# Performance work log

Hardware: AMD Instinct MI355X
Metric: run time of the kernel (lower is better)

Reference implementation:

```python
import jax, jax.numpy as jnp
import numpy as np

N_CLUSTERS = 16
N_ITERATIONS = 5
COV_INIT = 1.0


def setup_inputs() -> dict:
    key = jax.random.key(0)
    k1, k2 = jax.random.split(key)
    B, T, F, D = 8, 400, 256, 64
    data = jax.random.normal(k1, (B, T, F, D), dtype=jnp.float32)
    # Replicate init_means: per batch row, pick K random indices in [0, T),
    # offset by b*T, and gather rows of data flattened over (B,T,F).
    idx = jax.random.randint(k2, (B, N_CLUSTERS), 0, T)  # [B,K]
    idx = idx + jnp.arange(B)[:, None] * T
    flat = data.reshape(-1, D)  # [B*T*F, D]
    means = flat[idx.reshape(-1)].reshape(B, N_CLUSTERS, D)
    scale = jnp.ones((1,), dtype=jnp.float32)
    bias = jnp.zeros((1,), dtype=jnp.float32)
    return {"data": data, "means": means, "scale": scale, "bias": bias}


def _log_likelihoods(x, x2, means, var, pi):
    # x: [B,N,D], means/var: [B,K,D], pi: [B,K] -> lik: [B,K,N]
    inv = 1.0 / (var + 1e-6)
    # sum_d (x - m)^2 * inv, expanded into GEMM-friendly contractions
    dist = (jnp.einsum('bnd,bkd->bkn', x2, inv)
            - 2.0 * jnp.einsum('bnd,bkd->bkn', x, means * inv)
            + jnp.sum(means * means * inv, axis=-1)[:, :, None])
    coeff = -0.5 * jnp.sum(jnp.log(2.0 * np.pi * var), axis=-1)  # [B,K]
    return jnp.log(pi)[:, :, None] + coeff[:, :, None] - 0.5 * dist


def reference(data, means, scale, bias):
    B, T, F, D = data.shape
    K = means.shape[1]
    N = T * F
    x = data.reshape(B, N, D)
    x2 = x * x
    var = jnp.full((B, K, D), COV_INIT, dtype=data.dtype)
    pi = jnp.full((B, K), 1.0 / K, dtype=data.dtype)

    for _ in range(N_ITERATIONS):
        lik = _log_likelihoods(x, x2, means, var, pi)          # [B,K,N]
        post = jax.nn.softmax(lik, axis=1)                     # [B,K,N]
        cs = jnp.sum(post, axis=2)                             # [B,K]
        pi = cs / jnp.sum(cs, axis=1, keepdims=True)           # L1-normalized
        sx = jnp.einsum('bkn,bnd->bkd', post, x)               # [B,K,D]
        means = sx / (cs[:, :, None] + 1e-7)
        sx2 = jnp.einsum('bkn,bnd->bkd', post, x2)
        # sum_n post*(x - m)^2 = S(x^2) - 2 m S(x) + m^2 * cluster_size
        var = sx2 - 2.0 * means * sx + means * means * cs[:, :, None]
        var = var + 1e-6

    lik = _log_likelihoods(x, x2, means, var, pi)              # [B,K,N]
    lik = jnp.transpose(lik, (0, 2, 1)).reshape(B, T, F, K)
    return jax.nn.sigmoid(lik * scale[0] + bias[0])
```

## Files before the change

kernel.cpp:

```cpp
#include <hip/hip_runtime.h>
#include <math.h>

#define B_  8
#define T_  400
#define F_  256
#define D_  64
#define K_  16
#define N_  (T_*F_)
#define TILE 512
#define NBLK (N_/TILE)
#define PSTRIDE 20


__global__ void initk(const float* __restrict__ means_in,
                      float* __restrict__ means_s, float* __restrict__ var_s,
                      float* __restrict__ pi_s) {
    int i = blockIdx.x * 256 + threadIdx.x;
    if (i < B_*K_*D_) { means_s[i] = means_in[i]; var_s[i] = 1.0f; }
    if (i < B_*K_)    pi_s[i] = 1.0f / K_;
}

__global__ void prepk(const float* __restrict__ means_s, const float* __restrict__ var_s,
                      const float* __restrict__ pi_s,
                      float* __restrict__ pinv, float* __restrict__ pw,
                      float* __restrict__ pc0) {
    int bk = blockIdx.x;
    int d  = threadIdx.x;
    int idx = bk * D_ + d;
    float var = var_s[idx];
    float m   = means_s[idx];
    float inv = 1.0f / (var + 1e-6f);
    pinv[idx] = inv;
    pw[idx]   = m * inv;
    float r1 = logf(6.283185307179586f * var);
    float r2 = m * m * inv;
    #pragma unroll
    for (int off = 32; off > 0; off >>= 1) {
        r1 += __shfl_xor(r1, off);
        r2 += __shfl_xor(r2, off);
    }
    if (d == 0) pc0[bk] = logf(pi_s[bk]) - 0.5f * (r1 + r2);
}

__global__ __launch_bounds__(256, 3) void estepk(
        const float* __restrict__ xg,
        const float* __restrict__ pinv, const float* __restrict__ pw,
        const float* __restrict__ pc0,
        float* __restrict__ cs, float* __restrict__ sx, float* __restrict__ sx2) {
    __shared__ float pinv_lds[K_*D_];
    __shared__ float pw_lds[K_*D_];
    __shared__ float c0_lds[K_];
    __shared__ float post_lds[TILE * PSTRIDE];

    const int t  = threadIdx.x;
    const int b  = blockIdx.y;
    const int n0 = blockIdx.x * TILE;

    for (int i = t; i < K_*D_; i += 256) {
        pinv_lds[i] = pinv[b*K_*D_ + i];
        pw_lds[i]   = pw[b*K_*D_ + i];
    }
    if (t < K_) c0_lds[t] = pc0[b*K_ + t];
    __syncthreads();

    float t1a[16], t2a[16], t1b[16], t2b[16];
    #pragma unroll
    for (int k = 0; k < 16; ++k) { t1a[k]=0.f; t2a[k]=0.f; t1b[k]=0.f; t2b[k]=0.f; }

    const float4* pa = (const float4*)(xg + ((size_t)b*N_ + n0 + t) * D_);
    const float4* pb = pa + 256 * (D_/4);
    const float4* iv4 = (const float4*)pinv_lds;
    const float4* wv4 = (const float4*)pw_lds;

    #pragma unroll 2
    for (int c = 0; c < D_/4; ++c) {
        float4 xa = pa[c], xb = pb[c];
        float4 qa, qb;
        qa.x = xa.x*xa.x; qa.y = xa.y*xa.y; qa.z = xa.z*xa.z; qa.w = xa.w*xa.w;
        qb.x = xb.x*xb.x; qb.y = xb.y*xb.y; qb.z = xb.z*xb.z; qb.w = xb.w*xb.w;
        #pragma unroll
        for (int k = 0; k < 16; ++k) {
            float4 iv = iv4[k*16 + c];
            float4 wv = wv4[k*16 + c];
            t2a[k] = fmaf(qa.x, iv.x, fmaf(qa.y, iv.y, fmaf(qa.z, iv.z, fmaf(qa.w, iv.w, t2a[k]))));
            t1a[k] = fmaf(xa.x, wv.x, fmaf(xa.y, wv.y, fmaf(xa.z, wv.z, fmaf(xa.w, wv.w, t1a[k]))));
            t2b[k] = fmaf(qb.x, iv.x, fmaf(qb.y, iv.y, fmaf(qb.z, iv.z, fmaf(qb.w, iv.w, t2b[k]))));
            t1b[k] = fmaf(xb.x, wv.x, fmaf(xb.y, wv.y, fmaf(xb.z, wv.z, fmaf(xb.w, wv.w, t1b[k]))));
        }
    }

    {
        float lik[16]; float mx = -1e30f;
        #pragma unroll
        for (int k = 0; k < 16; ++k) { lik[k] = c0_lds[k] + t1a[k] - 0.5f*t2a[k]; mx = fmaxf(mx, lik[k]); }
        float s = 0.f;
        #pragma unroll
        for (int k = 0; k < 16; ++k) { lik[k] = __expf(lik[k] - mx); s += lik[k]; }
        float is = 1.0f / s;
        #pragma unroll
        for (int k = 0; k < 16; ++k) post_lds[t*PSTRIDE + k] = lik[k] * is;
    }
    {
        float lik[16]; float mx = -1e30f;
        #pragma unroll
        for (int k = 0; k < 16; ++k) { lik[k] = c0_lds[k] + t1b[k] - 0.5f*t2b[k]; mx = fmaxf(mx, lik[k]); }
        float s = 0.f;
        #pragma unroll
        for (int k = 0; k < 16; ++k) { lik[k] = __expf(lik[k] - mx); s += lik[k]; }
        float is = 1.0f / s;
        #pragma unroll
        for (int k = 0; k < 16; ++k) post_lds[(256 + t)*PSTRIDE + k] = lik[k] * is;
    }
    __syncthreads();

    const int lane = t & 63;
    const int kb   = (t >> 6) * 4;
    float sa[4]  = {0.f,0.f,0.f,0.f};
    float s2a[4] = {0.f,0.f,0.f,0.f};
    float ca[4]  = {0.f,0.f,0.f,0.f};
    const float* xrow = xg + ((size_t)b*N_ + n0) * D_ + lane;
    #pragma unroll 4
    for (int n = 0; n < TILE; ++n) {
        float xv = xrow[(size_t)n * D_];
        float4 p = *(const float4*)&post_lds[n*PSTRIDE + kb];
        float xx = xv * xv;
        ca[0] += p.x; ca[1] += p.y; ca[2] += p.z; ca[3] += p.w;
        sa[0] = fmaf(p.x, xv, sa[0]);  sa[1] = fmaf(p.y, xv, sa[1]);
        sa[2] = fmaf(p.z, xv, sa[2]);  sa[3] = fmaf(p.w, xv, sa[3]);
        s2a[0] = fmaf(p.x, xx, s2a[0]); s2a[1] = fmaf(p.y, xx, s2a[1]);
        s2a[2] = fmaf(p.z, xx, s2a[2]); s2a[3] = fmaf(p.w, xx, s2a[3]);
    }
    #pragma unroll
    for (int i = 0; i < 4; ++i) {
        atomicAdd(&sx [((size_t)b*K_ + kb + i)*D_ + lane], sa[i]);
        atomicAdd(&sx2[((size_t)b*K_ + kb + i)*D_ + lane], s2a[i]);
    }
    if (lane == 0) {
        #pragma unroll
        for (int i = 0; i < 4; ++i) atomicAdd(&cs[b*K_ + kb + i], ca[i]);
    }
}

__global__ void mstepk(float* __restrict__ means_s, float* __restrict__ var_s,
                       float* __restrict__ pi_s,
                       const float* __restrict__ cs, const float* __restrict__ sx,
                       const float* __restrict__ sx2) {
    int idx = blockIdx.x * 256 + threadIdx.x;
    int b = idx >> 10;
    int k = (idx >> 6) & 15;
    int d = idx & 63;
    float csv = cs[b*K_ + k];
    float sum = 0.f;
    #pragma unroll
    for (int j = 0; j < 16; ++j) sum += cs[b*K_ + j];
    float sxv = sx[idx], sx2v = sx2[idx];
    float mean = sxv / (csv + 1e-7f);
    float var  = fmaf(mean*mean, csv, fmaf(-2.0f*mean, sxv, sx2v)) + 1e-6f;
    means_s[idx] = mean;
    var_s[idx]   = var;
    if (d == 0) pi_s[b*K_ + k] = csv / sum;
}

__global__ __launch_bounds__(256, 3) void finalk(
        const float* __restrict__ xg,
        const float* __restrict__ pinv, const float* __restrict__ pw,
        const float* __restrict__ pc0,
        const float* __restrict__ scale, const float* __restrict__ bias,
        float* __restrict__ out) {
    __shared__ float pinv_lds[K_*D_];
    __shared__ float pw_lds[K_*D_];
    __shared__ float c0_lds[K_];

    const int t  = threadIdx.x;
    const int b  = blockIdx.y;
    const int n0 = blockIdx.x * TILE;

    for (int i = t; i < K_*D_; i += 256) {
        pinv_lds[i] = pinv[b*K_*D_ + i];
        pw_lds[i]   = pw[b*K_*D_ + i];
    }
    if (t < K_) c0_lds[t] = pc0[b*K_ + t];
    __syncthreads();

    float t1a[16], t2a[16], t1b[16], t2b[16];
    #pragma unroll
    for (int k = 0; k < 16; ++k) { t1a[k]=0.f; t2a[k]=0.f; t1b[k]=0.f; t2b[k]=0.f; }

    const float4* pa = (const float4*)(xg + ((size_t)b*N_ + n0 + t) * D_);
    const float4* pb = pa + 256 * (D_/4);
    const float4* iv4 = (const float4*)pinv_lds;
    const float4* wv4 = (const float4*)pw_lds;

    #pragma unroll 2
    for (int c = 0; c < D_/4; ++c) {
        float4 xa = pa[c], xb = pb[c];
        float4 qa, qb;
        qa.x = xa.x*xa.x; qa.y = xa.y*xa.y; qa.z = xa.z*xa.z; qa.w = xa.w*xa.w;
        qb.x = xb.x*xb.x; qb.y = xb.y*xb.y; qb.z = xb.z*xb.z; qb.w = xb.w*xb.w;
        #pragma unroll
        for (int k = 0; k < 16; ++k) {
            float4 iv = iv4[k*16 + c];
            float4 wv = wv4[k*16 + c];
            t2a[k] = fmaf(qa.x, iv.x, fmaf(qa.y, iv.y, fmaf(qa.z, iv.z, fmaf(qa.w, iv.w, t2a[k]))));
            t1a[k] = fmaf(xa.x, wv.x, fmaf(xa.y, wv.y, fmaf(xa.z, wv.z, fmaf(xa.w, wv.w, t1a[k]))));
            t2b[k] = fmaf(qb.x, iv.x, fmaf(qb.y, iv.y, fmaf(qb.z, iv.z, fmaf(qb.w, iv.w, t2b[k]))));
            t1b[k] = fmaf(xb.x, wv.x, fmaf(xb.y, wv.y, fmaf(xb.z, wv.z, fmaf(xb.w, wv.w, t1b[k]))));
        }
    }

    const float sc = scale[0], bi = bias[0];

    {
        float4* op = (float4*)(out + ((size_t)b*N_ + n0 + t) * (size_t)K_);
        #pragma unroll
        for (int q = 0; q < 4; ++q) {
            float4 o;
            float z0 = (c0_lds[4*q+0] + t1a[4*q+0] - 0.5f*t2a[4*q+0]) * sc + bi;
            float z1 = (c0_lds[4*q+1] + t1a[4*q+1] - 0.5f*t2a[4*q+1]) * sc + bi;
            float z2 = (c0_lds[4*q+2] + t1a[4*q+2] - 0.5f*t2a[4*q+2]) * sc + bi;
            float z3 = (c0_lds[4*q+3] + t1a[4*q+3] - 0.5f*t2a[4*q+3]) * sc + bi;
            o.x = 1.0f / (1.0f + __expf(-z0));
            o.y = 1.0f / (1.0f + __expf(-z1));
            o.z = 1.0f / (1.0f + __expf(-z2));
            o.w = 1.0f / (1.0f + __expf(-z3));
            op[q] = o;
        }
    }
    {
        float4* op = (float4*)(out + ((size_t)b*N_ + n0 + 256 + t) * (size_t)K_);
        #pragma unroll
        for (int q = 0; q < 4; ++q) {
            float4 o;
            float z0 = (c0_lds[4*q+0] + t1b[4*q+0] - 0.5f*t2b[4*q+0]) * sc + bi;
            float z1 = (c0_lds[4*q+1] + t1b[4*q+1] - 0.5f*t2b[4*q+1]) * sc + bi;
            float z2 = (c0_lds[4*q+2] + t1b[4*q+2] - 0.5f*t2b[4*q+2]) * sc + bi;
            float z3 = (c0_lds[4*q+3] + t1b[4*q+3] - 0.5f*t2b[4*q+3]) * sc + bi;
            o.x = 1.0f / (1.0f + __expf(-z0));
            o.y = 1.0f / (1.0f + __expf(-z1));
            o.z = 1.0f / (1.0f + __expf(-z2));
            o.w = 1.0f / (1.0f + __expf(-z3));
            op[q] = o;
        }
    }
}

extern "C" void kernel_launch(void* const* d_in, const int* in_sizes, int n_in,
                              void* d_out, int out_size, void* d_ws, size_t ws_size,
                              hipStream_t stream) {
    const float* xg       = (const float*)d_in[0];
    const float* means_in = (const float*)d_in[1];
    const float* scale    = (const float*)d_in[2];
    const float* bias     = (const float*)d_in[3];
    float* out = (float*)d_out;

    float* ws      = (float*)d_ws;
    float* means_s = ws + 0;
    float* var_s   = ws + 8192;
    float* pi_s    = ws + 16384;
    float* pinv    = ws + 16512;
    float* pw      = ws + 24704;
    float* pc0     = ws + 32896;
    float* cs      = ws + 33024;
    float* sx      = ws + 33152;
    float* sx2     = ws + 41344;

    initk<<<dim3(32), dim3(256), 0, stream>>>(means_in, means_s, var_s, pi_s);

    for (int it = 0; it < 5; ++it) {
        prepk<<<dim3(B_*K_), dim3(64), 0, stream>>>(means_s, var_s, pi_s, pinv, pw, pc0);
        hipMemsetAsync(cs, 0, (size_t)(128 + 8192 + 8192) * sizeof(float), stream);
        estepk<<<dim3(NBLK, B_), dim3(256), 0, stream>>>(xg, pinv, pw, pc0, cs, sx, sx2);
        mstepk<<<dim3(32), dim3(256), 0, stream>>>(means_s, var_s, pi_s, cs, sx, sx2);
    }
    prepk<<<dim3(B_*K_), dim3(64), 0, stream>>>(means_s, var_s, pi_s, pinv, pw, pc0);
    finalk<<<dim3(NBLK, B_), dim3(256), 0, stream>>>(xg, pinv, pw, pc0, scale, bias, out);
}
```

Baseline: 1.927 ms.

## Read cluster params from global memory and vectorize M-step accumulation with register tiling

The E-step and final kernels now read the per-batch inverse-variance and weighted-mean tables straight from global memory (uniform across the block, likely scalar or cache loads) instead of staging them in LDS, and keep the cluster constants in registers. Launch bounds rise to 4 blocks per SIMD. The accumulation phase now loads float4 rows of x, so each lane covers 4 dims by 4 clusters over strided rows, then combines partials with cross-lane shuffles before the atomics. This cuts LDS traffic and scalar global loads, at the cost of more registers and a shuffle reduction.

Result: faster. 1.733 ms (-10.1%).

```diff
diff --git a/kernel.cpp b/kernel.cpp
--- a/kernel.cpp
+++ b/kernel.cpp
@@ -9,7 +9,6 @@
 #define N_  (T_*F_)
 #define TILE 512
 #define NBLK (N_/TILE)
-#define PSTRIDE 20
 
 
 __global__ void initk(const float* __restrict__ means_in,
@@ -42,26 +41,23 @@
     if (d == 0) pc0[bk] = logf(pi_s[bk]) - 0.5f * (r1 + r2);
 }
 
-__global__ __launch_bounds__(256, 3) void estepk(
+__global__ __launch_bounds__(256, 4) void estepk(
         const float* __restrict__ xg,
         const float* __restrict__ pinv, const float* __restrict__ pw,
         const float* __restrict__ pc0,
         float* __restrict__ cs, float* __restrict__ sx, float* __restrict__ sx2) {
-    __shared__ float pinv_lds[K_*D_];
-    __shared__ float pw_lds[K_*D_];
-    __shared__ float c0_lds[K_];
-    __shared__ float post_lds[TILE * PSTRIDE];
+    __shared__ float post_lds[TILE * 16];
 
     const int t  = threadIdx.x;
     const int b  = blockIdx.y;
     const int n0 = blockIdx.x * TILE;
 
-    for (int i = t; i < K_*D_; i += 256) {
-        pinv_lds[i] = pinv[b*K_*D_ + i];
-        pw_lds[i]   = pw[b*K_*D_ + i];
-    }
-    if (t < K_) c0_lds[t] = pc0[b*K_ + t];
-    __syncthreads();
+    const float4* iv4 = (const float4*)(pinv + (size_t)(b*K_*D_));
+    const float4* wv4 = (const float4*)(pw   + (size_t)(b*K_*D_));
+
+    float c0r[16];
+    #pragma unroll
+    for (int k = 0; k < 16; ++k) c0r[k] = pc0[b*K_ + k];
 
     float t1a[16], t2a[16], t1b[16], t2b[16];
     #pragma unroll
@@ -69,8 +65,6 @@
 
     const float4* pa = (const float4*)(xg + ((size_t)b*N_ + n0 + t) * D_);
     const float4* pb = pa + 256 * (D_/4);
-    const float4* iv4 = (const float4*)pinv_lds;
-    const float4* wv4 = (const float4*)pw_lds;
 
     #pragma unroll 2
     for (int c = 0; c < D_/4; ++c) {
@@ -92,52 +86,89 @@
     {
         float lik[16]; float mx = -1e30f;
         #pragma unroll
-        for (int k = 0; k < 16; ++k) { lik[k] = c0_lds[k] + t1a[k] - 0.5f*t2a[k]; mx = fmaxf(mx, lik[k]); }
+        for (int k = 0; k < 16; ++k) { lik[k] = c0r[k] + t1a[k] - 0.5f*t2a[k]; mx = fmaxf(mx, lik[k]); }
         float s = 0.f;
         #pragma unroll
         for (int k = 0; k < 16; ++k) { lik[k] = __expf(lik[k] - mx); s += lik[k]; }
         float is = 1.0f / s;
         #pragma unroll
-        for (int k = 0; k < 16; ++k) post_lds[t*PSTRIDE + k] = lik[k] * is;
+        for (int k = 0; k < 16; ++k) post_lds[t*16 + k] = lik[k] * is;
     }
     {
         float lik[16]; float mx = -1e30f;
         #pragma unroll
-        for (int k = 0; k < 16; ++k) { lik[k] = c0_lds[k] + t1b[k] - 0.5f*t2b[k]; mx = fmaxf(mx, lik[k]); }
+        for (int k = 0; k < 16; ++k) { lik[k] = c0r[k] + t1b[k] - 0.5f*t2b[k]; mx = fmaxf(mx, lik[k]); }
         float s = 0.f;
         #pragma unroll
         for (int k = 0; k < 16; ++k) { lik[k] = __expf(lik[k] - mx); s += lik[k]; }
         float is = 1.0f / s;
         #pragma unroll
-        for (int k = 0; k < 16; ++k) post_lds[(256 + t)*PSTRIDE + k] = lik[k] * is;
+        for (int k = 0; k < 16; ++k) post_lds[(256 + t)*16 + k] = lik[k] * is;
     }
     __syncthreads();
 
     const int lane = t & 63;
     const int kb   = (t >> 6) * 4;
-    float sa[4]  = {0.f,0.f,0.f,0.f};
-    float s2a[4] = {0.f,0.f,0.f,0.f};
-    float ca[4]  = {0.f,0.f,0.f,0.f};
-    const float* xrow = xg + ((size_t)b*N_ + n0) * D_ + lane;
+    const int g    = lane & 15;
+    const int ps   = lane >> 4;
+
+    float sa[4][4], s2a[4][4], ca[4];
+    #pragma unroll
+    for (int i = 0; i < 4; ++i) {
+        ca[i] = 0.f;
+        #pragma unroll
+        for (int j = 0; j < 4; ++j) { sa[i][j] = 0.f; s2a[i][j] = 0.f; }
+    }
+
+    const float4* xq = (const float4*)(xg + ((size_t)b*N_ + n0) * D_);
+
     #pragma unroll 4
-    for (int n = 0; n < TILE; ++n) {
-        float xv = xrow[(size_t)n * D_];
-        float4 p = *(const float4*)&post_lds[n*PSTRIDE + kb];
-        float xx = xv * xv;
-        ca[0] += p.x; ca[1] += p.y; ca[2] += p.z; ca[3] += p.w;
-        sa[0] = fmaf(p.x, xv, sa[0]);  sa[1] = fmaf(p.y, xv, sa[1]);
-        sa[2] = fmaf(p.z, xv, sa[2]);  sa[3] = fmaf(p.w, xv, sa[3]);
-        s2a[0] = fmaf(p.x, xx, s2a[0]); s2a[1] = fmaf(p.y, xx, s2a[1]);
-        s2a[2] = fmaf(p.z, xx, s2a[2]); s2a[3] = fmaf(p.w, xx, s2a[3]);
-    }
-    #pragma unroll
-    for (int i = 0; i < 4; ++i) {
-        atomicAdd(&sx [((size_t)b*K_ + kb + i)*D_ + lane], sa[i]);
-        atomicAdd(&sx2[((size_t)b*K_ + kb + i)*D_ + lane], s2a[i]);
-    }
-    if (lane == 0) {
-        #pragma unroll
-        for (int i = 0; i < 4; ++i) atomicAdd(&cs[b*K_ + kb + i], ca[i]);
+    for (int n = 0; n < TILE; n += 4) {
+        const int p = n + ps;
+        float4 xv = xq[p*16 + g];
+        float4 pv = *(const float4*)&post_lds[p*16 + kb];
+        float xf[4] = {xv.x, xv.y, xv.z, xv.w};
+        float pf[4] = {pv.x, pv.y, pv.z, pv.w};
+        float qf[4];
+        #pragma unroll
+        for (int j = 0; j < 4; ++j) qf[j] = xf[j]*xf[j];
+        #pragma unroll
+        for (int i = 0; i < 4; ++i) {
+            ca[i] += pf[i];
+            #pragma unroll
+            for (int j = 0; j < 4; ++j) {
+                sa[i][j]  = fmaf(pf[i], xf[j], sa[i][j]);
+                s2a[i][j] = fmaf(pf[i], qf[j], s2a[i][j]);
+            }
+        }
+    }
+
+    #pragma unroll
+    for (int m = 16; m <= 32; m <<= 1) {
+        #pragma unroll
+        for (int i = 0; i < 4; ++i) {
+            ca[i] += __shfl_xor(ca[i], m);
+            #pragma unroll
+            for (int j = 0; j < 4; ++j) {
+                sa[i][j]  += __shfl_xor(sa[i][j],  m);
+                s2a[i][j] += __shfl_xor(s2a[i][j], m);
+            }
+        }
+    }
+
+    if (lane < 16) {
+        #pragma unroll
+        for (int i = 0; i < 4; ++i) {
+            #pragma unroll
+            for (int j = 0; j < 4; ++j) {
+                atomicAdd(&sx [((size_t)(b*K_ + kb + i))*D_ + 4*lane + j], sa[i][j]);
+                atomicAdd(&sx2[((size_t)(b*K_ + kb + i))*D_ + 4*lane + j], s2a[i][j]);
+            }
+        }
+        if (lane == 0) {
+            #pragma unroll
+            for (int i = 0; i < 4; ++i) atomicAdd(&cs[b*K_ + kb + i], ca[i]);
+        }
     }
 }
 
@@ -161,26 +192,22 @@
     if (d == 0) pi_s[b*K_ + k] = csv / sum;
 }
 
-__global__ __launch_bounds__(256, 3) void finalk(
+__global__ __launch_bounds__(256, 4) void finalk(
         const float* __restrict__ xg,
         const float* __restrict__ pinv, const float* __restrict__ pw,
         const float* __restrict__ pc0,
         const float* __restrict__ scale, const float* __restrict__ bias,
         float* __restrict__ out) {
-    __shared__ float pinv_lds[K_*D_];
-    __shared__ float pw_lds[K_*D_];
-    __shared__ float c0_lds[K_];
-
     const int t  = threadIdx.x;
     const int b  = blockIdx.y;
     const int n0 = blockIdx.x * TILE;
 
-    for (int i = t; i < K_*D_; i += 256) {
-        pinv_lds[i] = pinv[b*K_*D_ + i];
-        pw_lds[i]   = pw[b*K_*D_ + i];
-    }
-    if (t < K_) c0_lds[t] = pc0[b*K_ + t];
-    __syncthreads();
+    const float4* iv4 = (const float4*)(pinv + (size_t)(b*K_*D_));
+    const float4* wv4 = (const float4*)(pw   + (size_t)(b*K_*D_));
+
+    float c0r[16];
+    #pragma unroll
+    for (int k = 0; k < 16; ++k) c0r[k] = pc0[b*K_ + k];
 
     float t1a[16], t2a[16], t1b[16], t2b[16];
     #pragma unroll
@@ -188,8 +215,6 @@
 
     const float4* pa = (const float4*)(xg + ((size_t)b*N_ + n0 + t) * D_);
     const float4* pb = pa + 256 * (D_/4);
-    const float4* iv4 = (const float4*)pinv_lds;
-    const float4* wv4 = (const float4*)pw_lds;
 
     #pragma unroll 2
     for (int c = 0; c < D_/4; ++c) {
@@ -215,10 +240,10 @@
         #pragma unroll
         for (int q = 0; q < 4; ++q) {
             float4 o;
-            float z0 = (c0_lds[4*q+0] + t1a[4*q+0] - 0.5f*t2a[4*q+0]) * sc + bi;
-            float z1 = (c0_lds[4*q+1] + t1a[4*q+1] - 0.5f*t2a[4*q+1]) * sc + bi;
-            float z2 = (c0_lds[4*q+2] + t1a[4*q+2] - 0.5f*t2a[4*q+2]) * sc + bi;
-            float z3 = (c0_lds[4*q+3] + t1a[4*q+3] - 0.5f*t2a[4*q+3]) * sc + bi;
+            float z0 = (c0r[4*q+0] + t1a[4*q+0] - 0.5f*t2a[4*q+0]) * sc + bi;
+            float z1 = (c0r[4*q+1] + t1a[4*q+1] - 0.5f*t2a[4*q+1]) * sc + bi;
+            float z2 = (c0r[4*q+2] + t1a[4*q+2] - 0.5f*t2a[4*q+2]) * sc + bi;
+            float z3 = (c0r[4*q+3] + t1a[4*q+3] - 0.5f*t2a[4*q+3]) * sc + bi;
             o.x = 1.0f / (1.0f + __expf(-z0));
             o.y = 1.0f / (1.0f + __expf(-z1));
             o.z = 1.0f / (1.0f + __expf(-z2));
@@ -231,10 +256,10 @@
         #pragma unroll
         for (int q = 0; q < 4; ++q) {
             float4 o;
-            float z0 = (c0_lds[4*q+0] + t1b[4*q+0] - 0.5f*t2b[4*q+0]) * sc + bi;
-            float z1 = (c0_lds[4*q+1] + t1b[4*q+1] - 0.5f*t2b[4*q+1]) * sc + bi;
-            float z2 = (c0_lds[4*q+2] + t1b[4*q+2] - 0.5f*t2b[4*q+2]) * sc + bi;
-            float z3 = (c0_lds[4*q+3] + t1b[4*q+3] - 0.5f*t2b[4*q+3]) * sc + bi;
+            float z0 = (c0r[4*q+0] + t1b[4*q+0] - 0.5f*t2b[4*q+0]) * sc + bi;
+            float z1 = (c0r[4*q+1] + t1b[4*q+1] - 0.5f*t2b[4*q+1]) * sc + bi;
+            float z2 = (c0r[4*q+2] + t1b[4*q+2] - 0.5f*t2b[4*q+2]) * sc + bi;
+            float z3 = (c0r[4*q+3] + t1b[4*q+3] - 0.5f*t2b[4*q+3]) * sc + bi;
             o.x = 1.0f / (1.0f + __expf(-z0));
             o.y = 1.0f / (1.0f + __expf(-z1));
             o.z = 1.0f / (1.0f + __expf(-z2));
```
